# Optimization experiments

Measured on AMD Instinct MI355X. Metric: run time of the kernel, lower is better.

Reference implementation:

```python
import jax, jax.numpy as jnp
import numpy as np

INPUT_DIM = 1024
OUTPUT_DIM = 1024
DEGREE = 8


def setup_inputs() -> dict:
    key = jax.random.key(0)
    k1, k2 = jax.random.split(key)
    x = jax.random.normal(k1, (8192, INPUT_DIM), dtype=jnp.float32)
    std = 1.0 / (INPUT_DIM * (DEGREE + 1))
    cheby_coeffs = jax.random.normal(k2, (INPUT_DIM, OUTPUT_DIM, DEGREE + 1), dtype=jnp.float32) * std
    return {"x": x, "cheby_coeffs": cheby_coeffs}


def reference(x, cheby_coeffs):
    # x: [B, I]; cheby_coeffs: [I, O, D+1]
    degree = cheby_coeffs.shape[-1] - 1
    t = jnp.clip(jnp.tanh(x), -0.999, 0.999)            # [B, I]
    theta = jnp.arccos(t)[..., None]                     # [B, I, 1]
    arange = jnp.arange(degree + 1, dtype=x.dtype)       # [D+1]
    basis = jnp.cos(theta * arange)                      # [B, I, D+1] Chebyshev T_d(t)
    y = jnp.einsum('bid,iod->bo', basis, cheby_coeffs)   # [B, O]
    return y
```

## Files before the change

kernel.cpp:

```cpp
#include <hip/hip_runtime.h>
#include <stdint.h>

#define B_ROWS 8192
#define I_DIM  1024
#define N_DIM  1024
#define NDEG   9
#define K_DIM  (I_DIM * NDEG)

typedef __attribute__((ext_vector_type(8))) short  short8;
typedef __attribute__((ext_vector_type(4))) float  f32x4;

__device__ __forceinline__ unsigned short f2bf(float f) {
  union { float f; uint32_t u; } v; v.f = f;
  uint32_t u = v.u;
  u += 0x7FFFu + ((u >> 16) & 1u);
  return (unsigned short)(u >> 16);
}

__global__ __launch_bounds__(256) void basis_kernel(const float* __restrict__ x,
                                                    unsigned short* __restrict__ A) {
  const int b  = blockIdx.x;
  const int i0 = threadIdx.x * 4;
  const float4 xv = *reinterpret_cast<const float4*>(x + (size_t)b * I_DIM + i0);
  float t[4];
  t[0] = fminf(fmaxf(tanhf(xv.x), -0.999f), 0.999f);
  t[1] = fminf(fmaxf(tanhf(xv.y), -0.999f), 0.999f);
  t[2] = fminf(fmaxf(tanhf(xv.z), -0.999f), 0.999f);
  t[3] = fminf(fmaxf(tanhf(xv.w), -0.999f), 0.999f);

  unsigned short* outb = A + (size_t)b * K_DIM + i0;
  *reinterpret_cast<ushort4*>(outb) = make_ushort4(0x3F80u, 0x3F80u, 0x3F80u, 0x3F80u);

  float Tp[4] = {1.f, 1.f, 1.f, 1.f};
  float Tc[4] = {t[0], t[1], t[2], t[3]};
  #pragma unroll
  for (int d = 1; d < NDEG; ++d) {
    ushort4 o4;
    o4.x = f2bf(Tc[0]); o4.y = f2bf(Tc[1]); o4.z = f2bf(Tc[2]); o4.w = f2bf(Tc[3]);
    *reinterpret_cast<ushort4*>(outb + (size_t)d * I_DIM) = o4;
    if (d < NDEG - 1) {
      #pragma unroll
      for (int j = 0; j < 4; ++j) {
        float Tn = 2.0f * t[j] * Tc[j] - Tp[j];
        Tp[j] = Tc[j]; Tc[j] = Tn;
      }
    }
  }
}

__global__ __launch_bounds__(256) void repack_kernel(const float* __restrict__ cf,
                                                     unsigned short* __restrict__ Bt) {
  __shared__ unsigned short L[32][584];
  const int i0  = blockIdx.x * 32;
  const int o0  = blockIdx.y * 64;
  const int tid = threadIdx.x;

  #pragma unroll
  for (int j = 0; j < 18; ++j) {
    const int f4  = j * 256 + tid;
    const int il  = f4 / 144;
    const int odq = f4 % 144;
    const float4 v = *reinterpret_cast<const float4*>(
        cf + ((size_t)(i0 + il) * N_DIM + o0) * NDEG + (size_t)odq * 4);
    ushort4 w;
    w.x = f2bf(v.x); w.y = f2bf(v.y); w.z = f2bf(v.z); w.w = f2bf(v.w);
    *reinterpret_cast<ushort4*>(&L[il][odq * 4]) = w;
  }
  __syncthreads();

  for (int od = tid; od < 576; od += 256) {
    const int o = od / 9, d = od % 9;
    const size_t base = (size_t)(o0 + o) * K_DIM + (size_t)d * I_DIM + i0;
    #pragma unroll
    for (int ci = 0; ci < 4; ++ci) {
      uint32_t uu[4];
      #pragma unroll
      for (int p = 0; p < 4; ++p) {
        unsigned short lo = L[ci * 8 + p * 2 + 0][od];
        unsigned short hi = L[ci * 8 + p * 2 + 1][od];
        uu[p] = (uint32_t)lo | ((uint32_t)hi << 16);
      }
      uint4 u; u.x = uu[0]; u.y = uu[1]; u.z = uu[2]; u.w = uu[3];
      *reinterpret_cast<uint4*>(Bt + base + ci * 8) = u;
    }
  }
}

__global__ __launch_bounds__(256) void gemm_kernel(const unsigned short* __restrict__ A,
                                                   const unsigned short* __restrict__ Bt,
                                                   float* __restrict__ C) {
  __shared__ unsigned short As[128 * 64];
  __shared__ unsigned short Bs[128 * 64];
  const int tid  = threadIdx.x;
  const int lane = tid & 63;
  const int wave = tid >> 6;
  const int q    = lane >> 4;
  const int ml   = lane & 15;
  const int wm   = wave >> 1;
  const int wn   = wave & 1;
  const int n0   = blockIdx.x * 128;
  const int m0   = blockIdx.y * 128;

  const int sr   = tid >> 3;
  const int slot = tid & 7;

  f32x4 acc[4][4];
  #pragma unroll
  for (int a = 0; a < 4; ++a)
    #pragma unroll
    for (int b = 0; b < 4; ++b)
      acc[a][b] = f32x4{0.f, 0.f, 0.f, 0.f};

  for (int kt = 0; kt < K_DIM / 64; ++kt) {
    const int k0 = kt * 64;
    #pragma unroll
    for (int s = 0; s < 4; ++s) {
      const int r  = s * 32 + sr;
      const int gc = slot ^ (r & 7);
      const unsigned short* srcA = A + (size_t)(m0 + r) * K_DIM + k0 + gc * 8;
      __builtin_amdgcn_global_load_lds(
          (const __attribute__((address_space(1))) void*)srcA,
          (__attribute__((address_space(3))) void*)&As[r * 64 + slot * 8], 16, 0, 0);
      const unsigned short* srcB = Bt + (size_t)(n0 + r) * K_DIM + k0 + gc * 8;
      __builtin_amdgcn_global_load_lds(
          (const __attribute__((address_space(1))) void*)srcB,
          (__attribute__((address_space(3))) void*)&Bs[r * 64 + slot * 8], 16, 0, 0);
    }
    __syncthreads();

    #pragma unroll
    for (int ks = 0; ks < 2; ++ks) {
      short8 av[4], bv[4];
      #pragma unroll
      for (int mi = 0; mi < 4; ++mi) {
        const int row = wm * 64 + mi * 16 + ml;
        const int sl  = (ks * 4 + q) ^ (row & 7);
        av[mi] = *reinterpret_cast<const short8*>(&As[row * 64 + sl * 8]);
      }
      #pragma unroll
      for (int ni = 0; ni < 4; ++ni) {
        const int row = wn * 64 + ni * 16 + ml;
        const int sl  = (ks * 4 + q) ^ (row & 7);
        bv[ni] = *reinterpret_cast<const short8*>(&Bs[row * 64 + sl * 8]);
      }
      #pragma unroll
      for (int mi = 0; mi < 4; ++mi)
        #pragma unroll
        for (int ni = 0; ni < 4; ++ni)
          acc[mi][ni] = __builtin_amdgcn_mfma_f32_16x16x32_bf16(av[mi], bv[ni], acc[mi][ni], 0, 0, 0);
    }
    __syncthreads();
  }

  #pragma unroll
  for (int mi = 0; mi < 4; ++mi) {
    #pragma unroll
    for (int ni = 0; ni < 4; ++ni) {
      const int col = n0 + wn * 64 + ni * 16 + ml;
      #pragma unroll
      for (int r = 0; r < 4; ++r) {
        const int row = m0 + wm * 64 + mi * 16 + q * 4 + r;
        C[(size_t)row * N_DIM + col] = acc[mi][ni][r];
      }
    }
  }
}

extern "C" void kernel_launch(void* const* d_in, const int* in_sizes, int n_in,
                              void* d_out, int out_size, void* d_ws, size_t ws_size,
                              hipStream_t stream) {
  const float* x      = (const float*)d_in[0];
  const float* coeffs = (const float*)d_in[1];
  float* y            = (float*)d_out;

  const size_t bt_bytes = (size_t)N_DIM * K_DIM * sizeof(unsigned short);
  unsigned short* Bt = (unsigned short*)d_ws;
  unsigned short* A  = (unsigned short*)((char*)d_ws + bt_bytes);

  repack_kernel<<<dim3(I_DIM / 32, N_DIM / 64), 256, 0, stream>>>(coeffs, Bt);

  size_t avail    = (ws_size > bt_bytes) ? (ws_size - bt_bytes) : 0;
  size_t rows_fit = avail / ((size_t)K_DIM * sizeof(unsigned short));
  int m_chunk = (int)((rows_fit / 128) * 128);
  if (m_chunk > B_ROWS) m_chunk = B_ROWS;
  if (m_chunk < 128)    m_chunk = 128;

  for (int m0 = 0; m0 < B_ROWS; m0 += m_chunk) {
    int mc = B_ROWS - m0; if (mc > m_chunk) mc = m_chunk;
    basis_kernel<<<mc, 256, 0, stream>>>(x + (size_t)m0 * I_DIM, A);
    gemm_kernel<<<dim3(N_DIM / 128, mc / 128), 256, 0, stream>>>(
        A, Bt, y + (size_t)m0 * N_DIM);
  }
}
```

Before: 319.8 us.

## Fold constant T0 term into bias and split GEMM K dimension in two

Result: slower. 332.8 us (+4.1%).

```diff
diff --git a/kernel.cpp b/kernel.cpp
--- a/kernel.cpp
+++ b/kernel.cpp
@@ -5,7 +5,8 @@
 #define I_DIM  1024
 #define N_DIM  1024
 #define NDEG   9
-#define K_DIM  (I_DIM * NDEG)
+#define K_DIM  (I_DIM * (NDEG-1))
+#define K_HALF (K_DIM / 2)
 
 typedef __attribute__((ext_vector_type(8))) short  short8;
 typedef __attribute__((ext_vector_type(4))) float  f32x4;
@@ -15,6 +16,11 @@
   uint32_t u = v.u;
   u += 0x7FFFu + ((u >> 16) & 1u);
   return (unsigned short)(u >> 16);
+}
+
+__device__ __forceinline__ float bf2f(unsigned short h) {
+  union { uint32_t u; float f; } v; v.u = ((uint32_t)h) << 16;
+  return v.f;
 }
 
 __global__ __launch_bounds__(256) void basis_kernel(const float* __restrict__ x,
@@ -29,15 +35,13 @@
   t[3] = fminf(fmaxf(tanhf(xv.w), -0.999f), 0.999f);
 
   unsigned short* outb = A + (size_t)b * K_DIM + i0;
-  *reinterpret_cast<ushort4*>(outb) = make_ushort4(0x3F80u, 0x3F80u, 0x3F80u, 0x3F80u);
-
   float Tp[4] = {1.f, 1.f, 1.f, 1.f};
   float Tc[4] = {t[0], t[1], t[2], t[3]};
   #pragma unroll
   for (int d = 1; d < NDEG; ++d) {
     ushort4 o4;
     o4.x = f2bf(Tc[0]); o4.y = f2bf(Tc[1]); o4.z = f2bf(Tc[2]); o4.w = f2bf(Tc[3]);
-    *reinterpret_cast<ushort4*>(outb + (size_t)d * I_DIM) = o4;
+    *reinterpret_cast<ushort4*>(outb + (size_t)(d - 1) * I_DIM) = o4;
     if (d < NDEG - 1) {
       #pragma unroll
       for (int j = 0; j < 4; ++j) {
@@ -49,7 +53,8 @@
 }
 
 __global__ __launch_bounds__(256) void repack_kernel(const float* __restrict__ cf,
-                                                     unsigned short* __restrict__ Bt) {
+                                                     unsigned short* __restrict__ Bt,
+                                                     float* __restrict__ bias) {
   __shared__ unsigned short L[32][584];
   const int i0  = blockIdx.x * 32;
   const int o0  = blockIdx.y * 64;
@@ -70,20 +75,35 @@
 
   for (int od = tid; od < 576; od += 256) {
     const int o = od / 9, d = od % 9;
-    const size_t base = (size_t)(o0 + o) * K_DIM + (size_t)d * I_DIM + i0;
-    #pragma unroll
-    for (int ci = 0; ci < 4; ++ci) {
-      uint32_t uu[4];
-      #pragma unroll
-      for (int p = 0; p < 4; ++p) {
-        unsigned short lo = L[ci * 8 + p * 2 + 0][od];
-        unsigned short hi = L[ci * 8 + p * 2 + 1][od];
-        uu[p] = (uint32_t)lo | ((uint32_t)hi << 16);
-      }
-      uint4 u; u.x = uu[0]; u.y = uu[1]; u.z = uu[2]; u.w = uu[3];
-      *reinterpret_cast<uint4*>(Bt + base + ci * 8) = u;
-    }
-  }
+    if (d == 0) {
+      float s = 0.f;
+      #pragma unroll
+      for (int il = 0; il < 32; ++il) s += bf2f(L[il][od]);
+      atomicAdd(&bias[o0 + o], s);
+    } else {
+      const size_t base = (size_t)(o0 + o) * K_DIM + (size_t)(d - 1) * I_DIM + i0;
+      #pragma unroll
+      for (int ci = 0; ci < 4; ++ci) {
+        uint32_t uu[4];
+        #pragma unroll
+        for (int p = 0; p < 4; ++p) {
+          unsigned short lo = L[ci * 8 + p * 2 + 0][od];
+          unsigned short hi = L[ci * 8 + p * 2 + 1][od];
+          uu[p] = (uint32_t)lo | ((uint32_t)hi << 16);
+        }
+        uint4 u; u.x = uu[0]; u.y = uu[1]; u.z = uu[2]; u.w = uu[3];
+        *reinterpret_cast<uint4*>(Bt + base + ci * 8) = u;
+      }
+    }
+  }
+}
+
+__global__ __launch_bounds__(256) void init_out_kernel(const float* __restrict__ bias,
+                                                       float* __restrict__ C) {
+  const int b = blockIdx.x;
+  const int o = threadIdx.x * 4;
+  const float4 bv = *reinterpret_cast<const float4*>(bias + o);
+  *reinterpret_cast<float4*>(C + (size_t)b * N_DIM + o) = bv;
 }
 
 __global__ __launch_bounds__(256) void gemm_kernel(const unsigned short* __restrict__ A,
@@ -100,6 +120,7 @@
   const int wn   = wave & 1;
   const int n0   = blockIdx.x * 128;
   const int m0   = blockIdx.y * 128;
+  const int kz   = blockIdx.z;
 
   const int sr   = tid >> 3;
   const int slot = tid & 7;
@@ -111,7 +132,9 @@
     for (int b = 0; b < 4; ++b)
       acc[a][b] = f32x4{0.f, 0.f, 0.f, 0.f};
 
-  for (int kt = 0; kt < K_DIM / 64; ++kt) {
+  const int kt_beg = kz * (K_HALF / 64);
+  const int kt_end = kt_beg + (K_HALF / 64);
+  for (int kt = kt_beg; kt < kt_end; ++kt) {
     const int k0 = kt * 64;
     #pragma unroll
     for (int s = 0; s < 4; ++s) {
@@ -160,7 +183,7 @@
       #pragma unroll
       for (int r = 0; r < 4; ++r) {
         const int row = m0 + wm * 64 + mi * 16 + q * 4 + r;
-        C[(size_t)row * N_DIM + col] = acc[mi][ni][r];
+        atomicAdd(&C[(size_t)row * N_DIM + col], acc[mi][ni][r]);
       }
     }
   }
@@ -175,11 +198,16 @@
 
   const size_t bt_bytes = (size_t)N_DIM * K_DIM * sizeof(unsigned short);
   unsigned short* Bt = (unsigned short*)d_ws;
-  unsigned short* A  = (unsigned short*)((char*)d_ws + bt_bytes);
-
-  repack_kernel<<<dim3(I_DIM / 32, N_DIM / 64), 256, 0, stream>>>(coeffs, Bt);
-
-  size_t avail    = (ws_size > bt_bytes) ? (ws_size - bt_bytes) : 0;
+  float* bias        = (float*)((char*)d_ws + bt_bytes);
+  unsigned short* A  = (unsigned short*)((char*)d_ws + bt_bytes + 4096);
+
+  hipMemsetAsync(bias, 0, N_DIM * sizeof(float), stream);
+
+  repack_kernel<<<dim3(I_DIM / 32, N_DIM / 64), 256, 0, stream>>>(coeffs, Bt, bias);
+
+  init_out_kernel<<<B_ROWS, 256, 0, stream>>>(bias, y);
+
+  size_t avail    = (ws_size > bt_bytes + 4096) ? (ws_size - bt_bytes - 4096) : 0;
   size_t rows_fit = avail / ((size_t)K_DIM * sizeof(unsigned short));
   int m_chunk = (int)((rows_fit / 128) * 128);
   if (m_chunk > B_ROWS) m_chunk = B_ROWS;
@@ -188,7 +216,7 @@
   for (int m0 = 0; m0 < B_ROWS; m0 += m_chunk) {
     int mc = B_ROWS - m0; if (mc > m_chunk) mc = m_chunk;
     basis_kernel<<<mc, 256, 0, stream>>>(x + (size_t)m0 * I_DIM, A);
-    gemm_kernel<<<dim3(N_DIM / 128, mc / 128), 256, 0, stream>>>(
+    gemm_kernel<<<dim3(N_DIM / 128, mc / 128, 2), 256, 0, stream>>>(
         A, Bt, y + (size_t)m0 * N_DIM);
   }
 }
```
